# Kernel optimization log

Hardware: AMD Instinct MI355X
Metric: run time of the kernel (lower is better)

## Reference

```python
import jax, jax.numpy as jnp
import numpy as np

N, E, D_LM, H, L, C = 100000, 1000000, 1024, 128, 3, 8


def setup_inputs() -> dict:
    key = jax.random.key(0)
    ks = jax.random.split(key, 8)
    return {
        "last_hidden_state": jax.random.normal(ks[0], (N, D_LM), jnp.float32),
        "edge_index": jax.random.randint(ks[1], (2, E), 0, N, dtype=jnp.int32),
        "W_lm": jax.random.normal(ks[2], (D_LM, H), jnp.float32) * 0.03,
        "b_lm": jnp.zeros((H,), jnp.float32),
        "W_gcn": jax.random.normal(ks[3], (L, H, H), jnp.float32) * 0.08,
        "b_gcn": jnp.zeros((L, H), jnp.float32),
        "W_cls": jax.random.normal(ks[4], (2 * H, C), jnp.float32) * 0.06,
        "b_cls": jnp.zeros((C,), jnp.float32),
    }


def reference(last_hidden_state, edge_index, W_lm, b_lm, W_gcn, b_gcn, W_cls, b_cls):
    # Frozen LM output -> lm_head (dropout is identity in eval mode)
    n = last_hidden_state.shape[0]
    lm = last_hidden_state @ W_lm + b_lm                      # [N, H]

    # GCN normalization (add self-loops, symmetric deg^{-1/2} norm), shared by all layers
    loops = jnp.arange(n, dtype=edge_index.dtype)
    src = jnp.concatenate([edge_index[0], loops])             # message sources j
    dst = jnp.concatenate([edge_index[1], loops])             # aggregation targets i
    deg = jax.ops.segment_sum(jnp.ones_like(dst, jnp.float32), dst, num_segments=n)
    dinv = jax.lax.rsqrt(jnp.maximum(deg, 1.0))               # deg >= 1 due to self-loops
    norm = dinv[src] * dinv[dst]                              # [E+N]

    out = lm
    for l in range(W_gcn.shape[0]):
        h = out @ W_gcn[l]                                    # linear transform first (PyG GCNConv)
        msg = h[src] * norm[:, None]                          # gather + scale  [E+N, H]
        out = jax.ops.segment_sum(msg, dst, num_segments=n) + b_gcn[l]
        out = jax.nn.relu(out)                                # dropout identity in eval

    logits = jnp.concatenate([lm, out], axis=-1) @ W_cls + b_cls  # [N, C]
    return logits
```

## Files before the change

kernel.cpp:

```cpp
#include <hip/hip_runtime.h>


using bf16x8 = __attribute__((ext_vector_type(8))) short;
using f32x4  = __attribute__((ext_vector_type(4))) float;
typedef unsigned short u16;
typedef unsigned int   u32;

__device__ __forceinline__ u16 f2bf(float f) {
  u32 u = __builtin_bit_cast(u32, f);
  u += 0x7fffu + ((u >> 16) & 1u);
  return (u16)(u >> 16);
}
__device__ __forceinline__ float bf2f(u32 lo16) {
  return __builtin_bit_cast(float, lo16 << 16);
}
__device__ __forceinline__ u32 packbf2(float a, float b) {
  u32 r;
  asm("v_cvt_pk_bf16_f32 %0, %1, %2" : "=v"(r) : "v"(a), "v"(b));
  return r;
}
__device__ __forceinline__ void gl_lds16(const void* g, void* l) {
  __builtin_amdgcn_global_load_lds(
      (const __attribute__((address_space(1))) void*)g,
      (__attribute__((address_space(3))) void*)l, 16, 0, 0);
}


__global__ void count_kernel(const int* __restrict__ dst, int* __restrict__ counts, int E) {
  int e = blockIdx.x * 256 + threadIdx.x;
  if (e < E) atomicAdd(&counts[dst[e]], 1);
}

__global__ void dinv_kernel(const int* __restrict__ counts, float* __restrict__ dinv, int N) {
  int i = blockIdx.x * 256 + threadIdx.x;
  if (i < N) dinv[i] = rsqrtf((float)(counts[i] + 1));
}

__global__ void scan_partial(const int* __restrict__ counts, int* __restrict__ partials, int N) {
  __shared__ int sdata[256];
  int t = threadIdx.x;
  int base = blockIdx.x * 1024 + t * 4;
  int s = 0;
#pragma unroll
  for (int i = 0; i < 4; i++) { int idx = base + i; if (idx < N) s += counts[idx]; }
  sdata[t] = s; __syncthreads();
  for (int off = 128; off > 0; off >>= 1) {
    if (t < off) sdata[t] += sdata[t + off];
    __syncthreads();
  }
  if (t == 0) partials[blockIdx.x] = sdata[0];
}

__global__ void scan_partials_excl(int* __restrict__ partials, int NB,
                                   int* __restrict__ offsets, int N, int E) {
  __shared__ int sdata[256];
  int t = threadIdx.x;
  int v = (t < NB) ? partials[t] : 0;
  sdata[t] = v; __syncthreads();
  int val = v;
  for (int off = 1; off < 256; off <<= 1) {
    int add = (t >= off) ? sdata[t - off] : 0;
    __syncthreads();
    val += add; sdata[t] = val;
    __syncthreads();
  }
  if (t < NB) partials[t] = val - v;
  if (t == 0) offsets[N] = E;
}

__global__ void scan_final(const int* __restrict__ counts, const int* __restrict__ partials,
                           int* __restrict__ offsets, int N) {
  __shared__ int sdata[256];
  int t = threadIdx.x;
  int base = blockIdx.x * 1024 + t * 4;
  int v[4]; int tsum = 0;
#pragma unroll
  for (int i = 0; i < 4; i++) { int idx = base + i; v[i] = (idx < N) ? counts[idx] : 0; tsum += v[i]; }
  sdata[t] = tsum; __syncthreads();
  int val = tsum;
  for (int off = 1; off < 256; off <<= 1) {
    int add = (t >= off) ? sdata[t - off] : 0;
    __syncthreads();
    val += add; sdata[t] = val;
    __syncthreads();
  }
  int run = partials[blockIdx.x] + val - tsum;
#pragma unroll
  for (int i = 0; i < 4; i++) { int idx = base + i; if (idx < N) offsets[idx] = run; run += v[i]; }
}

__global__ void fill_kernel(const int* __restrict__ src, const int* __restrict__ dst,
                            const int* __restrict__ offsets, int* __restrict__ cursor,
                            int* __restrict__ col, int E) {
  int e = blockIdx.x * 256 + threadIdx.x;
  if (e < E) {
    int d = dst[e];
    int p = offsets[d] + atomicAdd(&cursor[d], 1);
    col[p] = src[e];
  }
}


__global__ void prep_wlm(const float* __restrict__ W, u16* __restrict__ Wt) {
  int idx = blockIdx.x * 256 + threadIdx.x;
  if (idx < 1024 * 128) {
    int k = idx >> 7, c = idx & 127;
    Wt[c * 1024 + k] = f2bf(W[idx]);
  }
}
__global__ void prep_wgcn(const float* __restrict__ W, u16* __restrict__ Wt, int total) {
  int idx = blockIdx.x * 256 + threadIdx.x;
  if (idx < total) {
    int l = idx >> 14; int r = idx & 16383;
    int k = r >> 7, c = r & 127;
    Wt[l * 16384 + c * 128 + k] = f2bf(W[idx]);
  }
}


__global__ __launch_bounds__(256) void gemm_lm_kernel(
    const float* __restrict__ A, const u16* __restrict__ Bt,
    const float* __restrict__ bias, u16* __restrict__ Out, int Nrows)
{
  __shared__ u16 lA[128 * 32];
  __shared__ u16 lB[128 * 32];
  const int t = threadIdx.x;
  const int lane = t & 63;
  const int w = t >> 6;
  const int wr = w >> 1, wc = w & 1;
  const int row0 = blockIdx.x * 128;
  const int quad = lane >> 4;
  const int l16 = lane & 15;

  f32x4 acc[4][4];
#pragma unroll
  for (int i = 0; i < 4; i++)
#pragma unroll
    for (int j = 0; j < 4; j++) acc[i][j] = f32x4{0.f, 0.f, 0.f, 0.f};

  for (int k0 = 0; k0 < 1024; k0 += 32) {
#pragma unroll
    for (int rpt = 0; rpt < 2; rpt++) {
      int seg = t + rpt * 256;
      int c = seg >> 2;
      int ch = (seg & 3) ^ (c & 3);
      gl_lds16((const char*)Bt + (size_t)c * 2048 + (size_t)k0 * 2 + ch * 16,
               (char*)lB + seg * 16);
    }
#pragma unroll
    for (int rpt = 0; rpt < 2; rpt++) {
      int seg = t + rpt * 256;
      int row = seg >> 2, ks = seg & 3;
      int grow = row0 + row; if (grow >= Nrows) grow = Nrows - 1;
      const float* gp = A + (size_t)grow * 1024 + k0 + ks * 8;
      float4 f0 = *reinterpret_cast<const float4*>(gp);
      float4 f1 = *reinterpret_cast<const float4*>(gp + 4);
      uint4 pk;
      pk.x = packbf2(f0.x, f0.y); pk.y = packbf2(f0.z, f0.w);
      pk.z = packbf2(f1.x, f1.y); pk.w = packbf2(f1.z, f1.w);
      *reinterpret_cast<uint4*>((char*)lA + ((seg * 16) ^ ((row & 3) << 4))) = pk;
    }
    __syncthreads();

    bf16x8 af[4], bfr[4];
#pragma unroll
    for (int i = 0; i < 4; i++) {
      int r = wr * 64 + i * 16 + l16;
      af[i] = *reinterpret_cast<const bf16x8*>(
          (const char*)lA + r * 64 + ((quad ^ (r & 3)) << 4));
    }
#pragma unroll
    for (int j = 0; j < 4; j++) {
      int c = wc * 64 + j * 16 + l16;
      bfr[j] = *reinterpret_cast<const bf16x8*>(
          (const char*)lB + c * 64 + ((quad ^ (c & 3)) << 4));
    }
    __syncthreads();

#pragma unroll
    for (int i = 0; i < 4; i++)
#pragma unroll
      for (int j = 0; j < 4; j++)
        acc[i][j] = __builtin_amdgcn_mfma_f32_16x16x32_bf16(af[i], bfr[j], acc[i][j], 0, 0, 0);
  }

#pragma unroll
  for (int i = 0; i < 4; i++) {
    int rbase = row0 + wr * 64 + i * 16 + quad * 4;
#pragma unroll
    for (int j = 0; j < 4; j++) {
      int c = wc * 64 + j * 16 + l16;
      float bv = bias[c];
#pragma unroll
      for (int r = 0; r < 4; r++) {
        int grow = rbase + r;
        if (grow < Nrows)
          Out[(size_t)grow * 128 + c] = f2bf(acc[i][j][r] + bv);
      }
    }
  }
}


__global__ __launch_bounds__(256) void gemm128_kernel(
    const u16* __restrict__ A, const u16* __restrict__ Bt,
    const float* __restrict__ rs, u16* __restrict__ Out, int Nrows)
{
  __shared__ u16 lA[128 * 128];
  __shared__ u16 lB[128 * 128];
  const int t = threadIdx.x;
  const int lane = t & 63;
  const int w = t >> 6;
  const int wr = w >> 1, wc = w & 1;
  const int row0 = blockIdx.x * 128;
  const int quad = lane >> 4;
  const int l16 = lane & 15;

#pragma unroll
  for (int rp = 0; rp < 8; rp++) {
    int o = (t + rp * 256) * 16;
    int row = o >> 8;
    int io = (o ^ ((row & 15) << 4)) & 255;
    long grow = (long)row0 + row;
    if (grow >= Nrows) grow = Nrows - 1;
    gl_lds16((const char*)A + grow * 256 + io, (char*)lA + o);
    gl_lds16((const char*)Bt + row * 256 + io, (char*)lB + o);
  }
  __syncthreads();

  f32x4 acc[4][4];
#pragma unroll
  for (int i = 0; i < 4; i++)
#pragma unroll
    for (int j = 0; j < 4; j++) acc[i][j] = f32x4{0.f, 0.f, 0.f, 0.f};

#pragma unroll
  for (int kk = 0; kk < 4; kk++) {
    bf16x8 af[4], bfr[4];
#pragma unroll
    for (int i = 0; i < 4; i++) {
      int r = wr * 64 + i * 16 + l16;
      int ch = (kk * 4 + quad) ^ (r & 15);
      af[i] = *reinterpret_cast<const bf16x8*>((const char*)lA + r * 256 + ch * 16);
    }
#pragma unroll
    for (int j = 0; j < 4; j++) {
      int c = wc * 64 + j * 16 + l16;
      int ch = (kk * 4 + quad) ^ (c & 15);
      bfr[j] = *reinterpret_cast<const bf16x8*>((const char*)lB + c * 256 + ch * 16);
    }
#pragma unroll
    for (int i = 0; i < 4; i++)
#pragma unroll
      for (int j = 0; j < 4; j++)
        acc[i][j] = __builtin_amdgcn_mfma_f32_16x16x32_bf16(af[i], bfr[j], acc[i][j], 0, 0, 0);
  }

#pragma unroll
  for (int i = 0; i < 4; i++) {
    int rbase = row0 + wr * 64 + i * 16 + quad * 4;
#pragma unroll
    for (int r = 0; r < 4; r++) {
      int grow = rbase + r;
      if (grow < Nrows) {
        float sc = rs[grow];
#pragma unroll
        for (int j = 0; j < 4; j++) {
          int c = wc * 64 + j * 16 + l16;
          Out[(size_t)grow * 128 + c] = f2bf(acc[i][j][r] * sc);
        }
      }
    }
  }
}


#define BRED(v) do { v += __shfl_xor(v, 1);  v += __shfl_xor(v, 2);  v += __shfl_xor(v, 4); \
                     v += __shfl_xor(v, 8);  v += __shfl_xor(v, 16); v += __shfl_xor(v, 32); } while (0)

template<bool FINAL>
__global__ __launch_bounds__(256) void aggregate_kernel(
    const u16* __restrict__ h, const int* __restrict__ offsets,
    const int* __restrict__ col, const float* __restrict__ dinv,
    const float* __restrict__ bias, u16* __restrict__ outf,
    const u16* __restrict__ lm, const float* __restrict__ Wc,
    const float* __restrict__ bc, float* __restrict__ logits, int N)
{
  int w = threadIdx.x >> 6;
  int lane = threadIdx.x & 63;
  int i = blockIdx.x * 4 + w;
  if (i >= N) return;
  const u32* h32 = (const u32*)h;
  u32 us = h32[(size_t)i * 64 + lane];
  float ax = bf2f(us & 0xffffu), ay = bf2f(us >> 16);
  int s = offsets[i], e = offsets[i + 1];
  for (int base = s; base < e; base += 64) {
    int cnt = e - base; if (cnt > 64) cnt = 64;
    int cj = (base + lane < e) ? col[base + lane] : 0;
    int k = 0;
    for (; k + 4 <= cnt; k += 4) {
      int j0 = __shfl(cj, k),     j1 = __shfl(cj, k + 1);
      int j2 = __shfl(cj, k + 2), j3 = __shfl(cj, k + 3);
      u32 u0 = h32[(size_t)j0 * 64 + lane];
      u32 u1 = h32[(size_t)j1 * 64 + lane];
      u32 u2 = h32[(size_t)j2 * 64 + lane];
      u32 u3 = h32[(size_t)j3 * 64 + lane];
      ax += bf2f(u0 & 0xffffu); ay += bf2f(u0 >> 16);
      ax += bf2f(u1 & 0xffffu); ay += bf2f(u1 >> 16);
      ax += bf2f(u2 & 0xffffu); ay += bf2f(u2 >> 16);
      ax += bf2f(u3 & 0xffffu); ay += bf2f(u3 >> 16);
    }
    for (; k < cnt; k++) {
      int j = __shfl(cj, k);
      u32 uu = h32[(size_t)j * 64 + lane];
      ax += bf2f(uu & 0xffffu); ay += bf2f(uu >> 16);
    }
  }
  float di = dinv[i];
  ax = fmaxf(ax * di + bias[lane * 2], 0.f);
  ay = fmaxf(ay * di + bias[lane * 2 + 1], 0.f);
  if (!FINAL) {
    ((u32*)outf)[(size_t)i * 64 + lane] = packbf2(ax, ay);
  } else {
    u32 ul = ((const u32*)lm)[(size_t)i * 64 + lane];
    float lx = bf2f(ul & 0xffffu), ly = bf2f(ul >> 16);
    const float4* W4 = (const float4*)Wc;
    float4 a0 = W4[(2 * lane) * 2],       a1 = W4[(2 * lane) * 2 + 1];
    float4 b0 = W4[(2 * lane + 1) * 2],   b1 = W4[(2 * lane + 1) * 2 + 1];
    float4 c0 = W4[(128 + 2 * lane) * 2], c1 = W4[(128 + 2 * lane) * 2 + 1];
    float4 d0 = W4[(129 + 2 * lane) * 2], d1 = W4[(129 + 2 * lane) * 2 + 1];
    float s0 = lx * a0.x + ly * b0.x + ax * c0.x + ay * d0.x;
    float s1 = lx * a0.y + ly * b0.y + ax * c0.y + ay * d0.y;
    float s2 = lx * a0.z + ly * b0.z + ax * c0.z + ay * d0.z;
    float s3 = lx * a0.w + ly * b0.w + ax * c0.w + ay * d0.w;
    float s4 = lx * a1.x + ly * b1.x + ax * c1.x + ay * d1.x;
    float s5 = lx * a1.y + ly * b1.y + ax * c1.y + ay * d1.y;
    float s6 = lx * a1.z + ly * b1.z + ax * c1.z + ay * d1.z;
    float s7 = lx * a1.w + ly * b1.w + ax * c1.w + ay * d1.w;
    BRED(s0); BRED(s1); BRED(s2); BRED(s3); BRED(s4); BRED(s5); BRED(s6); BRED(s7);
    if (lane < 8) {
      float v = s0;
      v = (lane == 1) ? s1 : v;
      v = (lane == 2) ? s2 : v;
      v = (lane == 3) ? s3 : v;
      v = (lane == 4) ? s4 : v;
      v = (lane == 5) ? s5 : v;
      v = (lane == 6) ? s6 : v;
      v = (lane == 7) ? s7 : v;
      logits[(size_t)i * 8 + lane] = v + bc[lane];
    }
  }
}
#undef BRED


static inline char* bump(char*& p, size_t bytes) {
  char* r = p;
  p += (bytes + 255) & ~(size_t)255;
  return r;
}

extern "C" void kernel_launch(void* const* d_in, const int* in_sizes, int n_in,
                              void* d_out, int out_size, void* d_ws, size_t ws_size,
                              hipStream_t stream) {
  const float* X   = (const float*)d_in[0];
  const int*   EI  = (const int*)  d_in[1];
  const float* Wlm = (const float*)d_in[2];
  const float* blm = (const float*)d_in[3];
  const float* Wg  = (const float*)d_in[4];
  const float* bg  = (const float*)d_in[5];
  const float* Wc  = (const float*)d_in[6];
  const float* bc  = (const float*)d_in[7];
  float* out = (float*)d_out;

  const int N = in_sizes[0] / 1024;
  const int E = in_sizes[1] / 2;
  const int L = in_sizes[4] / (128 * 128);

  char* wp = (char*)d_ws;
  int*   counts  = (int*)  bump(wp, (size_t)N * 4);
  int*   cursor  = (int*)  bump(wp, (size_t)N * 4);
  int*   offs    = (int*)  bump(wp, (size_t)(N + 1) * 4);
  float* dinv    = (float*)bump(wp, (size_t)N * 4);
  int*   partials= (int*)  bump(wp, 1024 * 4);
  int*   colA    = (int*)  bump(wp, (size_t)E * 4);
  u16*   WlmT    = (u16*)  bump(wp, (size_t)1024 * 128 * 2);
  u16*   WgT     = (u16*)  bump(wp, (size_t)L * 128 * 128 * 2);
  u16*   lmB     = (u16*)  bump(wp, (size_t)N * 128 * 2);
  u16*   hB      = (u16*)  bump(wp, (size_t)N * 128 * 2);
  u16*   featB   = (u16*)  bump(wp, (size_t)N * 128 * 2);

  hipMemsetAsync(counts, 0, (size_t)N * 4, stream);
  hipMemsetAsync(cursor, 0, (size_t)N * 4, stream);

  const int* srcp = EI;
  const int* dstp = EI + E;

  count_kernel<<<(E + 255) / 256, 256, 0, stream>>>(dstp, counts, E);
  dinv_kernel<<<(N + 255) / 256, 256, 0, stream>>>(counts, dinv, N);

  int NB = (N + 1023) / 1024;
  scan_partial<<<NB, 256, 0, stream>>>(counts, partials, N);
  scan_partials_excl<<<1, 256, 0, stream>>>(partials, NB, offs, N, E);
  scan_final<<<NB, 256, 0, stream>>>(counts, partials, offs, N);
  fill_kernel<<<(E + 255) / 256, 256, 0, stream>>>(srcp, dstp, offs, cursor, colA, E);

  prep_wlm<<<(1024 * 128 + 255) / 256, 256, 0, stream>>>(Wlm, WlmT);
  prep_wgcn<<<(L * 128 * 128 + 255) / 256, 256, 0, stream>>>(Wg, WgT, L * 128 * 128);

  int GB = (N + 127) / 128;
  gemm_lm_kernel<<<GB, 256, 0, stream>>>(X, WlmT, blm, lmB, N);

  const u16* cur = lmB;
  for (int l = 0; l < L; l++) {
    gemm128_kernel<<<GB, 256, 0, stream>>>(cur, WgT + (size_t)l * 16384, dinv, hB, N);
    if (l < L - 1) {
      aggregate_kernel<false><<<(N + 3) / 4, 256, 0, stream>>>(
          hB, offs, colA, dinv, bg + (size_t)l * 128, featB,
          nullptr, nullptr, nullptr, nullptr, N);
      cur = featB;
    } else {
      aggregate_kernel<true><<<(N + 3) / 4, 256, 0, stream>>>(
          hB, offs, colA, dinv, bg + (size_t)l * 128, nullptr,
          lmB, Wc, bc, out, N);
    }
  }
}
```

Measured before the change: 950.1 us.

## Double-buffer LM-head GEMM with register prefetch and reuse counts as fill cursor

The LM-head GEMM now uses double-buffered LDS tiles. The next B tile is loaded asynchronously into the alternate buffer, A tiles are prefetched two steps ahead into registers, and one barrier per k-step replaces the two syncthreads. The goal is to overlap the fp32 A-matrix streaming with MFMA work in this memory-bound GEMM, at the cost of more registers and LDS. Separately, the CSR fill decrements the counts array instead of incrementing a separate cursor, which removes one memset and buffer. This assumes nothing reads counts after the fill (dinv is computed earlier).

```diff
diff --git a/kernel.cpp b/kernel.cpp
--- a/kernel.cpp
+++ b/kernel.cpp
@@ -90,12 +90,12 @@
 }
 
 __global__ void fill_kernel(const int* __restrict__ src, const int* __restrict__ dst,
-                            const int* __restrict__ offsets, int* __restrict__ cursor,
+                            const int* __restrict__ offsets, int* __restrict__ counts,
                             int* __restrict__ col, int E) {
   int e = blockIdx.x * 256 + threadIdx.x;
   if (e < E) {
     int d = dst[e];
-    int p = offsets[d] + atomicAdd(&cursor[d], 1);
+    int p = offsets[d] + atomicSub(&counts[d], 1) - 1;
     col[p] = src[e];
   }
 }
@@ -122,78 +122,138 @@
     const float* __restrict__ A, const u16* __restrict__ Bt,
     const float* __restrict__ bias, u16* __restrict__ Out, int Nrows)
 {
-  __shared__ u16 lA[128 * 32];
-  __shared__ u16 lB[128 * 32];
+  __shared__ u16 lA[2][128 * 32];
+  __shared__ u16 lB[2][128 * 32];
   const int t = threadIdx.x;
   const int lane = t & 63;
   const int w = t >> 6;
   const int wr = w >> 1, wc = w & 1;
-  const int row0 = blockIdx.x * 128;
+  const long rowbase = (long)blockIdx.x * 128;
   const int quad = lane >> 4;
   const int l16 = lane & 15;
 
+  const int seg0 = t, seg1 = t + 256;
+  const int r0 = seg0 >> 2, kq0 = seg0 & 3;
+  const int r1 = seg1 >> 2, kq1 = seg1 & 3;
+  long g0 = rowbase + r0; if (g0 >= Nrows) g0 = Nrows - 1;
+  long g1 = rowbase + r1; if (g1 >= Nrows) g1 = Nrows - 1;
+  const float* Ab0 = A + g0 * 1024 + kq0 * 8;
+  const float* Ab1 = A + g1 * 1024 + kq1 * 8;
+  const int dA0 = (seg0 * 16) ^ ((r0 & 3) << 4);
+  const int dA1 = (seg1 * 16) ^ ((r1 & 3) << 4);
+  const char* Bsrc0 = (const char*)Bt + (size_t)r0 * 2048 + ((kq0 ^ (r0 & 3)) << 4);
+  const char* Bsrc1 = (const char*)Bt + (size_t)r1 * 2048 + ((kq1 ^ (r1 & 3)) << 4);
+  const int dB0 = seg0 * 16, dB1 = seg1 * 16;
+
   f32x4 acc[4][4];
 #pragma unroll
   for (int i = 0; i < 4; i++)
 #pragma unroll
     for (int j = 0; j < 4; j++) acc[i][j] = f32x4{0.f, 0.f, 0.f, 0.f};
 
-  for (int k0 = 0; k0 < 1024; k0 += 32) {
-#pragma unroll
-    for (int rpt = 0; rpt < 2; rpt++) {
-      int seg = t + rpt * 256;
-      int c = seg >> 2;
-      int ch = (seg & 3) ^ (c & 3);
-      gl_lds16((const char*)Bt + (size_t)c * 2048 + (size_t)k0 * 2 + ch * 16,
-               (char*)lB + seg * 16);
-    }
-#pragma unroll
-    for (int rpt = 0; rpt < 2; rpt++) {
-      int seg = t + rpt * 256;
-      int row = seg >> 2, ks = seg & 3;
-      int grow = row0 + row; if (grow >= Nrows) grow = Nrows - 1;
-      const float* gp = A + (size_t)grow * 1024 + k0 + ks * 8;
-      float4 f0 = *reinterpret_cast<const float4*>(gp);
-      float4 f1 = *reinterpret_cast<const float4*>(gp + 4);
-      uint4 pk;
-      pk.x = packbf2(f0.x, f0.y); pk.y = packbf2(f0.z, f0.w);
-      pk.z = packbf2(f1.x, f1.y); pk.w = packbf2(f1.z, f1.w);
-      *reinterpret_cast<uint4*>((char*)lA + ((seg * 16) ^ ((row & 3) << 4))) = pk;
-    }
-    __syncthreads();
-
+  float4 fa[2][4];
+
+#define GLB(KS, BUF) do { \
+    gl_lds16(Bsrc0 + (size_t)(KS) * 64, (char*)lB[BUF] + dB0); \
+    gl_lds16(Bsrc1 + (size_t)(KS) * 64, (char*)lB[BUF] + dB1); \
+  } while (0)
+
+#define ALOAD(KS, S) do { \
+    fa[S][0] = *reinterpret_cast<const float4*>(Ab0 + (KS) * 32); \
+    fa[S][1] = *reinterpret_cast<const float4*>(Ab0 + (KS) * 32 + 4); \
+    fa[S][2] = *reinterpret_cast<const float4*>(Ab1 + (KS) * 32); \
+    fa[S][3] = *reinterpret_cast<const float4*>(Ab1 + (KS) * 32 + 4); \
+  } while (0)
+
+#define APACK(S, BUF) do { \
+    uint4 pk0, pk1; \
+    pk0.x = packbf2(fa[S][0].x, fa[S][0].y); pk0.y = packbf2(fa[S][0].z, fa[S][0].w); \
+    pk0.z = packbf2(fa[S][1].x, fa[S][1].y); pk0.w = packbf2(fa[S][1].z, fa[S][1].w); \
+    pk1.x = packbf2(fa[S][2].x, fa[S][2].y); pk1.y = packbf2(fa[S][2].z, fa[S][2].w); \
+    pk1.z = packbf2(fa[S][3].x, fa[S][3].y); pk1.w = packbf2(fa[S][3].z, fa[S][3].w); \
+    *reinterpret_cast<uint4*>((char*)lA[BUF] + dA0) = pk0; \
+    *reinterpret_cast<uint4*>((char*)lA[BUF] + dA1) = pk1; \
+  } while (0)
+
+#define FRAGS(BUF) do { \
+    _Pragma("unroll") \
+    for (int i = 0; i < 4; i++) { \
+      int r = wr * 64 + i * 16 + l16; \
+      af[i] = *reinterpret_cast<const bf16x8*>( \
+          (const char*)lA[BUF] + r * 64 + ((quad ^ (r & 3)) << 4)); \
+    } \
+    _Pragma("unroll") \
+    for (int j = 0; j < 4; j++) { \
+      int c = wc * 64 + j * 16 + l16; \
+      bfr[j] = *reinterpret_cast<const bf16x8*>( \
+          (const char*)lB[BUF] + c * 64 + ((quad ^ (c & 3)) << 4)); \
+    } \
+  } while (0)
+
+#define MFMA16() do { \
+    _Pragma("unroll") \
+    for (int i = 0; i < 4; i++) \
+      _Pragma("unroll") \
+      for (int j = 0; j < 4; j++) \
+        acc[i][j] = __builtin_amdgcn_mfma_f32_16x16x32_bf16(af[i], bfr[j], acc[i][j], 0, 0, 0); \
+  } while (0)
+
+  GLB(0, 0);
+  ALOAD(0, 0);
+  ALOAD(1, 1);
+  APACK(0, 0);
+  asm volatile("s_waitcnt vmcnt(0) lgkmcnt(0)" ::: "memory");
+  __builtin_amdgcn_s_barrier();
+  __builtin_amdgcn_sched_barrier(0);
+
+#define STEP_FULL(KS, BUF, SPACK, SLOAD) do { \
+    bf16x8 af[4], bfr[4]; \
+    FRAGS(BUF); \
+    GLB((KS) + 1, BUF ^ 1); \
+    APACK(SPACK, BUF ^ 1); \
+    ALOAD((KS) + 2, SLOAD); \
+    MFMA16(); \
+    asm volatile("s_waitcnt vmcnt(4) lgkmcnt(0)" ::: "memory"); \
+    __builtin_amdgcn_s_barrier(); \
+    __builtin_amdgcn_sched_barrier(0); \
+  } while (0)
+
+  for (int ks = 0; ks < 30; ks += 2) {
+    STEP_FULL(ks, 0, 1, 0);
+    STEP_FULL(ks + 1, 1, 0, 1);
+  }
+  {
     bf16x8 af[4], bfr[4];
-#pragma unroll
-    for (int i = 0; i < 4; i++) {
-      int r = wr * 64 + i * 16 + l16;
-      af[i] = *reinterpret_cast<const bf16x8*>(
-          (const char*)lA + r * 64 + ((quad ^ (r & 3)) << 4));
-    }
-#pragma unroll
-    for (int j = 0; j < 4; j++) {
-      int c = wc * 64 + j * 16 + l16;
-      bfr[j] = *reinterpret_cast<const bf16x8*>(
-          (const char*)lB + c * 64 + ((quad ^ (c & 3)) << 4));
-    }
-    __syncthreads();
-
-#pragma unroll
-    for (int i = 0; i < 4; i++)
-#pragma unroll
-      for (int j = 0; j < 4; j++)
-        acc[i][j] = __builtin_amdgcn_mfma_f32_16x16x32_bf16(af[i], bfr[j], acc[i][j], 0, 0, 0);
-  }
+    FRAGS(0);
+    GLB(31, 1);
+    APACK(1, 1);
+    MFMA16();
+    asm volatile("s_waitcnt vmcnt(0) lgkmcnt(0)" ::: "memory");
+    __builtin_amdgcn_s_barrier();
+    __builtin_amdgcn_sched_barrier(0);
+  }
+  {
+    bf16x8 af[4], bfr[4];
+    FRAGS(1);
+    MFMA16();
+  }
+#undef STEP_FULL
+#undef MFMA16
+#undef FRAGS
+#undef APACK
+#undef ALOAD
+#undef GLB
 
 #pragma unroll
   for (int i = 0; i < 4; i++) {
-    int rbase = row0 + wr * 64 + i * 16 + quad * 4;
+    long rbase = rowbase + wr * 64 + i * 16 + quad * 4;
 #pragma unroll
     for (int j = 0; j < 4; j++) {
       int c = wc * 64 + j * 16 + l16;
       float bv = bias[c];
 #pragma unroll
       for (int r = 0; r < 4; r++) {
-        int grow = rbase + r;
+        long grow = rbase + r;
         if (grow < Nrows)
           Out[(size_t)grow * 128 + c] = f2bf(acc[i][j][r] + bv);
       }
@@ -379,7 +439,6 @@
 
   char* wp = (char*)d_ws;
   int*   counts  = (int*)  bump(wp, (size_t)N * 4);
-  int*   cursor  = (int*)  bump(wp, (size_t)N * 4);
   int*   offs    = (int*)  bump(wp, (size_t)(N + 1) * 4);
   float* dinv    = (float*)bump(wp, (size_t)N * 4);
   int*   partials= (int*)  bump(wp, 1024 * 4);
@@ -391,7 +450,6 @@
   u16*   featB   = (u16*)  bump(wp, (size_t)N * 128 * 2);
 
   hipMemsetAsync(counts, 0, (size_t)N * 4, stream);
-  hipMemsetAsync(cursor, 0, (size_t)N * 4, stream);
 
   const int* srcp = EI;
   const int* dstp = EI + E;
@@ -403,7 +461,7 @@
   scan_partial<<<NB, 256, 0, stream>>>(counts, partials, N);
   scan_partials_excl<<<1, 256, 0, stream>>>(partials, NB, offs, N, E);
   scan_final<<<NB, 256, 0, stream>>>(counts, partials, offs, N);
-  fill_kernel<<<(E + 255) / 256, 256, 0, stream>>>(srcp, dstp, offs, cursor, colA, E);
+  fill_kernel<<<(E + 255) / 256, 256, 0, stream>>>(srcp, dstp, offs, counts, colA, E);
 
   prep_wlm<<<(1024 * 128 + 255) / 256, 256, 0, stream>>>(Wlm, WlmT);
   prep_wgcn<<<(L * 128 * 128 + 255) / 256, 256, 0, stream>>>(Wg, WgT, L * 128 * 128);
```

New measurement: 938.3 us. About the same (-1.2%).
